# Kernel tuning notes

Hardware: AMD Instinct MI355X
Metric: run time of the kernel (lower is better)

Reference implementation:

```python
import jax, jax.numpy as jnp
import numpy as np
import math

D_MODEL = 2048
D_STATE = 64
D_CONV = 4
EXPAND = 2
HEADDIM = 128
NGROUPS = 1
CHUNK = 256
D_INNER = EXPAND * D_MODEL            # 4096
NHEADS = D_INNER // HEADDIM           # 32
CONV_DIM = D_INNER + 2 * NGROUPS * D_STATE   # 4224
D_IN_PROJ = 2 * D_INNER + 2 * NGROUPS * D_STATE + NHEADS  # 8352
BATCH, SEQLEN = 2, 4096
EPS = 1e-5


def segsum(x):
    # x: (..., T) -> (..., T, T) with s[i, j] = sum_{k=j+1}^{i} x[k], -inf above diag
    T = x.shape[-1]
    xx = jnp.broadcast_to(x[..., :, None], x.shape + (T,))
    mask_lo = jnp.tril(jnp.ones((T, T), dtype=bool), -1)
    xx = jnp.where(mask_lo, xx, 0.0)
    s = jnp.cumsum(xx, axis=-2)
    mask = jnp.tril(jnp.ones((T, T), dtype=bool), 0)
    return jnp.where(mask, s, -jnp.inf)


def ssd(X, A, B, C, block_len):
    # X:(b,L,h,p)  A:(b,L,h)  B,C:(b,L,h,n)
    b, L, h, p = X.shape
    c = L // block_len
    X = X.reshape(b, c, block_len, h, p)
    A = A.reshape(b, c, block_len, h).transpose(0, 3, 1, 2)  # b h c l
    B = B.reshape(b, c, block_len, h, -1)
    C = C.reshape(b, c, block_len, h, -1)
    A_cumsum = jnp.cumsum(A, axis=-1)
    Lmat = jnp.exp(segsum(A))                                  # b h c l l
    Y_diag = jnp.einsum('bclhn,bcshn,bhcls,bcshp->bclhp', C, B, Lmat, X)
    decay_states = jnp.exp(A_cumsum[:, :, :, -1:] - A_cumsum)  # b h c l
    states = jnp.einsum('bclhn,bhcl,bclhp->bchpn', B, decay_states, X)
    init = jnp.zeros_like(states[:, :1])
    states = jnp.concatenate([init, states], axis=1)
    decay_chunk = jnp.exp(segsum(jnp.pad(A_cumsum[:, :, :, -1], ((0, 0), (0, 0), (1, 0)))))
    new_states = jnp.einsum('bhzc,bchpn->bzhpn', decay_chunk, states)
    states, final_state = new_states[:, :-1], new_states[:, -1]
    Y_off = jnp.einsum('bclhn,bchpn,bhcl->bclhp', C, states, jnp.exp(A_cumsum))
    Y = (Y_diag + Y_off).reshape(b, L, h, p)
    return Y, final_state


def causal_dwconv(x, w, b):
    # x:(B,L,C)  w:(C,K) depthwise kernel  b:(C,)  -> causal conv, length preserved
    C, K = w.shape
    y = jax.lax.conv_general_dilated(
        x.transpose(0, 2, 1), w[:, None, :], (1,), [(K - 1, 0)],
        feature_group_count=C)
    return y.transpose(0, 2, 1) + b


def setup_inputs() -> dict:
    key = jax.random.key(0)
    ks = jax.random.split(key, 8)
    u = jax.random.normal(ks[0], (BATCH, SEQLEN, D_MODEL), dtype=jnp.float32)
    W_in = jax.random.normal(ks[1], (D_MODEL, D_IN_PROJ), dtype=jnp.float32) / np.sqrt(D_MODEL)
    conv_w = jax.random.normal(ks[2], (CONV_DIM, D_CONV), dtype=jnp.float32) / np.sqrt(D_CONV)
    conv_b = jnp.zeros((CONV_DIM,), dtype=jnp.float32)
    # dt_bias init: inverse-softplus of dt sampled log-uniform in [dt_min, dt_max]
    dt_min, dt_max, dt_floor = 1e-3, 1e-1, 1e-4
    dt = jnp.exp(jax.random.uniform(ks[3], (NHEADS,)) * (math.log(dt_max) - math.log(dt_min)) + math.log(dt_min))
    dt = jnp.clip(dt, dt_floor)
    dt_bias = dt + jnp.log(-jnp.expm1(-dt))
    A_log = jnp.log(jax.random.uniform(ks[4], (NHEADS,), minval=1.0, maxval=16.0))
    D = jnp.ones((NHEADS,), dtype=jnp.float32)
    norm_w = jnp.ones((D_INNER,), dtype=jnp.float32)
    W_out = jax.random.normal(ks[5], (D_INNER, D_MODEL), dtype=jnp.float32) / np.sqrt(D_INNER)
    return {"u": u, "W_in": W_in, "conv_w": conv_w, "conv_b": conv_b,
            "dt_bias": dt_bias, "A_log": A_log, "D": D, "norm_w": norm_w, "W_out": W_out}


def reference(u, W_in, conv_w, conv_b, dt_bias, A_log, D, norm_w, W_out):
    batch, seqlen, _ = u.shape
    zxbcdt = u @ W_in                                   # (B,L,8352)
    z, xBC, dt = jnp.split(zxbcdt, [D_INNER, D_INNER + CONV_DIM], axis=-1)
    dt = jax.nn.softplus(dt + dt_bias)                  # (B,L,H)
    xBC = jax.nn.silu(causal_dwconv(xBC, conv_w, conv_b))
    x, B, C = jnp.split(xBC, [D_INNER, D_INNER + NGROUPS * D_STATE], axis=-1)
    x = x.reshape(batch, seqlen, NHEADS, HEADDIM)
    B = jnp.broadcast_to(B.reshape(batch, seqlen, NGROUPS, D_STATE), (batch, seqlen, NHEADS, D_STATE))
    C = jnp.broadcast_to(C.reshape(batch, seqlen, NGROUPS, D_STATE), (batch, seqlen, NHEADS, D_STATE))
    A = -jnp.exp(A_log)                                 # (H,)
    x_scaled = x * dt[..., None]
    A_dt = A * dt                                       # (B,L,H)
    y, _final = ssd(x_scaled, A_dt, B, C, CHUNK)
    y = y.reshape(batch, seqlen, D_INNER)
    x_flat = x.reshape(batch, seqlen, D_INNER)
    D_full = jnp.repeat(D, HEADDIM)
    y = y + x_flat * D_full
    # gated RMSNorm, norm AFTER gate (norm_before_gate=False)
    yg = y * jax.nn.silu(z)
    var = jnp.mean(yg * yg, axis=-1, keepdims=True)
    y = yg * jax.lax.rsqrt(var + EPS) * norm_w
    return y @ W_out
```

## Files before the change

kernel.cpp:

```cpp
#include <hip/hip_runtime.h>

typedef short s8v __attribute__((ext_vector_type(8)));
typedef float f4v __attribute__((ext_vector_type(4)));
typedef unsigned short bfu;

#define MFMA16 __builtin_amdgcn_mfma_f32_16x16x32_bf16

constexpr int kSEQ = 4096;
constexpr int kBL  = 8192;
constexpr int kDM  = 2048;
constexpr int kDP  = 8352;
constexpr int kDPpad = 8448;
constexpr int kDI  = 4096;
constexpr int kCV  = 4224;
constexpr int kXBC = 4256;
constexpr int kNH  = 32;
constexpr int kHD  = 128;
constexpr int kDS  = 64;
constexpr int kCH  = 256;

#if defined(__has_builtin)
#  if __has_builtin(__builtin_amdgcn_global_load_lds)
#    define HAS_GLD 1
#  endif
#endif
#ifndef HAS_GLD
#  define HAS_GLD 0
#endif

__device__ __forceinline__ void gld_lds16(const void* g, void* lbase, int lane){
#if HAS_GLD
  (void)lane;
  __builtin_amdgcn_global_load_lds(
      (const __attribute__((address_space(1))) void*)g,
      (__attribute__((address_space(3))) void*)lbase, 16, 0, 0);
#else
  *(uint4*)((char*)lbase + lane * 16) = *(const uint4*)g;
#endif
}

__device__ __forceinline__ bfu f2bf(float f){
  union { float f; unsigned u; } c; c.f = f;
  return (bfu)((c.u + 0x7fffu + ((c.u >> 16) & 1u)) >> 16);
}
__device__ __forceinline__ float bf2f(bfu s){
  union { unsigned u; float f; } c; c.u = ((unsigned)s) << 16;
  return c.f;
}

__device__ __forceinline__ s8v frag_ld(const char* lds, int rowbase, int kh, int lane){
  int r = rowbase + (lane & 15);
  int slot = (kh << 2) + (lane >> 4);
  return *(const s8v*)(lds + (((r << 3) + (slot ^ (r & 7))) << 4));
}

__global__ __launch_bounds__(256) void k_zero(bfu* __restrict__ p, int n){
  int i = blockIdx.x * 256 + threadIdx.x;
  if (i < n) p[i] = 0;
}

__global__ __launch_bounds__(256) void k_cvt(const float* __restrict__ s, bfu* __restrict__ d, int n8){
  int i = blockIdx.x * 256 + threadIdx.x;
  int stride = gridDim.x * 256;
  for (; i < n8; i += stride){
    const float4* sp = (const float4*)(s + (size_t)i * 8);
    float4 a = sp[0], b = sp[1];
    uint4 pk; bfu* pp = (bfu*)&pk;
    pp[0]=f2bf(a.x); pp[1]=f2bf(a.y); pp[2]=f2bf(a.z); pp[3]=f2bf(a.w);
    pp[4]=f2bf(b.x); pp[5]=f2bf(b.y); pp[6]=f2bf(b.z); pp[7]=f2bf(b.w);
    *(uint4*)(d + (size_t)i * 8) = pk;
  }
}

__global__ __launch_bounds__(256) void k_transpose(const float* __restrict__ src, bfu* __restrict__ dst, int R, int C){
  __shared__ float tile[32][33];
  int c0 = blockIdx.x * 32, r0 = blockIdx.y * 32;
  int tx = threadIdx.x, ty = threadIdx.y;
  #pragma unroll
  for (int i = ty; i < 32; i += 8){
    int r = r0 + i, cc = c0 + tx;
    tile[i][tx] = (r < R && cc < C) ? src[(size_t)r * C + cc] : 0.f;
  }
  __syncthreads();
  #pragma unroll
  for (int i = ty; i < 32; i += 8){
    int dr = c0 + i, dc = r0 + tx;
    if (dr < C && dc < R) dst[(size_t)dr * R + dc] = f2bf(tile[tx][i]);
  }
}

template<int MODE>
__global__ __launch_bounds__(512, 2) void k_gemm256(const bfu* __restrict__ A, const bfu* __restrict__ Bt,
                                                    float* __restrict__ outF, bfu* __restrict__ outZ,
                                                    bfu* __restrict__ outX, int tilesN, int N, int K){
  extern __shared__ char lds[];
  int t = threadIdx.x, lane = t & 63, wave = t >> 6;
  int wr = wave >> 2, wc = wave & 3;
  int nwg = gridDim.x;
  int bid = blockIdx.x;
  int cpx = nwg >> 3;
  int wg = (bid & 7) * cpx + (bid >> 3);
  int tmTile = wg / tilesN, tnTile = wg % tilesN;
  int tm = tmTile << 8, tn = tnTile << 8;
  const bfu* Ab = A + (size_t)tm * K;
  const bfu* Bb = Bt + (size_t)tn * K;

  #define AU(b,kh) ((b) * 65536 + (kh) * 16384)
  #define BU(b,kh) ((b) * 65536 + 32768 + (kh) * 16384)

  auto stage_unit = [&](const bfu* srcbase, int unitOfs, int kcol0){
    #pragma unroll
    for (int j = 0; j < 2; ++j){
      int lg = j * 512 + wave * 64 + lane;
      int r = lg >> 2;
      int s = (lg & 3) ^ ((r >> 1) & 3);
      gld_lds16(srcbase + (size_t)r * K + kcol0 + s * 8,
                lds + unitOfs + (j * 512 + wave * 64) * 16, lane);
    }
  };
  auto rd_frag = [&](int unitOfs, int rbase) -> s8v {
    int r = rbase + (lane & 15);
    int s = lane >> 4;
    int g = (r << 2) + (s ^ ((r >> 1) & 3));
    return *(const s8v*)(lds + unitOfs + (g << 4));
  };

  f4v acc[8][4];
  f4v zz = {0.f, 0.f, 0.f, 0.f};
  #pragma unroll
  for (int m = 0; m < 8; ++m)
    #pragma unroll
    for (int n = 0; n < 4; ++n) acc[m][n] = zz;

  int nt = K >> 6;
  stage_unit(Ab, AU(0,0), 0);
  stage_unit(Bb, BU(0,0), 0);
  stage_unit(Ab, AU(0,1), 32);
  stage_unit(Bb, BU(0,1), 32);
  __builtin_amdgcn_sched_barrier(0);
  asm volatile("s_waitcnt vmcnt(4)" ::: "memory");
  __builtin_amdgcn_sched_barrier(0);
  __builtin_amdgcn_s_barrier();
  __builtin_amdgcn_sched_barrier(0);

  #pragma unroll 1
  for (int tt = 0; tt < nt; ++tt){
    int cb = tt & 1, nb = cb ^ 1;
    int k0n = (tt + 1) << 6;
    bool more = (tt + 1 < nt);
    #pragma unroll
    for (int kh = 0; kh < 2; ++kh){
      if (more){
        stage_unit(Ab, AU(nb,kh), k0n + kh * 32);
        stage_unit(Bb, BU(nb,kh), k0n + kh * 32);
      }
      s8v af[8], bf[4];
      #pragma unroll
      for (int m = 0; m < 8; ++m) af[m] = rd_frag(AU(cb,kh), wr * 128 + m * 16);
      #pragma unroll
      for (int n = 0; n < 4; ++n) bf[n] = rd_frag(BU(cb,kh), wc * 64 + n * 16);
      __builtin_amdgcn_s_setprio(1);
      #pragma unroll
      for (int n = 0; n < 4; ++n)
        #pragma unroll
        for (int m = 0; m < 8; ++m)
          acc[m][n] = MFMA16(af[m], bf[n], acc[m][n], 0, 0, 0);
      __builtin_amdgcn_s_setprio(0);
      __builtin_amdgcn_sched_barrier(0);
      asm volatile("s_waitcnt vmcnt(4)" ::: "memory");
      __builtin_amdgcn_sched_barrier(0);
      __builtin_amdgcn_s_barrier();
      __builtin_amdgcn_sched_barrier(0);
    }
  }

  int r0 = (lane >> 4) << 2;
  if (MODE == 0){
    #pragma unroll
    for (int m = 0; m < 8; ++m)
      #pragma unroll
      for (int n = 0; n < 4; ++n)
        #pragma unroll
        for (int r = 0; r < 4; ++r){
          size_t rg = (size_t)(tm + wr * 128 + m * 16 + r0 + r);
          int cg = tn + wc * 64 + n * 16 + (lane & 15);
          outF[rg * N + cg] = acc[m][n][r];
        }
  } else {
    #pragma unroll
    for (int m = 0; m < 8; ++m)
      #pragma unroll
      for (int n = 0; n < 4; ++n){
        int col = wc * 64 + n * 16 + (lane & 15);
        int cs = col >> 3, cl = col & 7;
        #pragma unroll
        for (int r = 0; r < 4; ++r){
          int row = wr * 128 + m * 16 + r0 + r;
          *(bfu*)(lds + row * 512 + ((cs ^ (row & 7)) << 4) + cl * 2) = f2bf(acc[m][n][r]);
        }
      }
    __syncthreads();
    bfu* op; int ldo, cofs;
    if (tn < 4096){ op = outZ; ldo = 4096; cofs = 0; }
    else          { op = outX; ldo = kXBC; cofs = 4096; }
    int row = t >> 1, half = t & 1;
    bfu* baseo = op + (size_t)(tm + row) * ldo + (tn - cofs) + half * 128;
    #pragma unroll
    for (int i = 0; i < 16; ++i){
      int cg = tn + half * 128 + i * 8;
      if (cg < kDP){
        uint4 v = *(const uint4*)(lds + row * 512 + (((half * 16 + i) ^ (row & 7)) << 4));
        *(uint4*)(baseo + i * 8) = v;
      }
    }
  }
  #undef AU
  #undef BU
}

__global__ __launch_bounds__(256) void k_conv(const bfu* __restrict__ xbc, const float* __restrict__ cw,
    const float* __restrict__ cb, bfu* __restrict__ xT,
    bfu* __restrict__ B16o, bfu* __restrict__ BTo, bfu* __restrict__ C16o){
  int cht = blockIdx.x;
  int lt = blockIdx.y;
  int b = lt >> 6;
  int l0 = (lt & 63) << 6;
  int t = threadIdx.x;
  __shared__ float w[256];
  __shared__ float bias[64];
  __shared__ bfu in16[67][66];
  __shared__ bfu out16[64][66];
  if (t < 64) bias[t] = cb[cht * 64 + t];
  w[t] = cw[cht * 256 + t];
  int chbase = cht * 64;
  for (int i = t; i < 67 * 64; i += 256){
    int rrow = i >> 6, cc = i & 63;
    int l = l0 + rrow - 3;
    bfu hv = 0;
    if (l >= 0) hv = xbc[((size_t)b * kSEQ + l) * kXBC + chbase + cc];
    in16[rrow][cc] = hv;
  }
  __syncthreads();
  for (int i = t; i < 4096; i += 256){
    int lr = i >> 6, cc = i & 63;
    float acc = bias[cc];
    #pragma unroll
    for (int j = 0; j < 4; ++j)
      acc += bf2f(in16[lr + j][cc]) * w[cc * 4 + j];
    float sv = acc / (1.f + __expf(-acc));
    out16[lr][cc] = f2bf(sv);
  }
  __syncthreads();
  if (chbase >= 4096){
    for (int i = t; i < 4096; i += 256){
      int lr = i >> 6, cc = i & 63;
      size_t row = (size_t)b * kSEQ + l0 + lr;
      int ch = chbase + cc;
      bfu v = out16[lr][cc];
      if (ch < 4096 + kDS) B16o[row * kDS + (ch - 4096)] = v;
      else                 C16o[row * kDS + (ch - 4096 - kDS)] = v;
    }
  }
  if (chbase < 4096 + kDS){
    for (int i = t; i < 4096; i += 256){
      int cc = i >> 6, lr = i & 63;
      int ch = chbase + cc;
      int lg = l0 + lr;
      bfu v = out16[lr][cc];
      if (ch < 4096){
        int hh = ch >> 7, p = ch & 127;
        xT[(((size_t)b * kNH + hh) * kHD + p) * kSEQ + lg] = v;
      } else if (ch < 4096 + kDS){
        BTo[((size_t)b * kDS + (ch - 4096)) * kSEQ + lg] = v;
      }
    }
  }
}

__global__ __launch_bounds__(256) void k_dtscan(const bfu* __restrict__ xbc, const float* __restrict__ dt_bias,
    const float* __restrict__ A_log, float* __restrict__ dtf, float* __restrict__ acum){
  int bi = blockIdx.x;
  int h = bi & 31, c = (bi >> 5) & 15, b = bi >> 9;
  int t = threadIdx.x;
  size_t row = (size_t)b * kSEQ + c * kCH + t;
  float draw = bf2f(xbc[row * kXBC + kCV + h]) + dt_bias[h];
  float dt = (draw > 20.f) ? draw : log1pf(__expf(draw));
  dtf[row * kNH + h] = dt;
  float dA = -__expf(A_log[h]) * dt;
  __shared__ float s[256];
  s[t] = dA;
  __syncthreads();
  #pragma unroll
  for (int off = 1; off < 256; off <<= 1){
    float v = (t >= off) ? s[t - off] : 0.f;
    __syncthreads();
    s[t] += v;
    __syncthreads();
  }
  acum[(size_t)bi * 256 + t] = s[t];
}

__global__ __launch_bounds__(256) void k_states(const bfu* __restrict__ xT, const bfu* __restrict__ BT,
    const float* __restrict__ dtf, const float* __restrict__ acum, bfu* __restrict__ states){
  int bi = blockIdx.x;
  int h = bi & 31, c = (bi >> 5) & 15, b = bi >> 9;
  int t = threadIdx.x, lane = t & 63, wave = t >> 6;
  int wr = wave >> 1, wc = wave & 1;
  __shared__ uint4 ldsX4[1024];
  __shared__ uint4 ldsB4[512];
  __shared__ float dsv[256];
  char* ldsX = (char*)ldsX4;
  char* ldsB = (char*)ldsB4;
  float Atot = acum[(size_t)bi * 256 + 255];
  {
    size_t row = (size_t)b * kSEQ + c * kCH + t;
    dsv[t] = dtf[row * kNH + h] * __expf(Atot - acum[(size_t)bi * 256 + t]);
  }
  f4v zz = {0.f, 0.f, 0.f, 0.f};
  f4v acc[4][2];
  #pragma unroll
  for (int m = 0; m < 4; ++m){ acc[m][0] = zz; acc[m][1] = zz; }
  const bfu* xTp = xT + ((size_t)b * kNH + h) * kHD * kSEQ + c * kCH;
  const bfu* BTp = BT + (size_t)b * kDS * kSEQ + c * kCH;
  __syncthreads();
  for (int kb = 0; kb < 4; ++kb){
    #pragma unroll
    for (int it = 0; it < 4; ++it){
      int s = it * 256 + t;
      int row = s >> 3;
      int srcslot = (s & 7) ^ (row & 7);
      gld_lds16(xTp + (size_t)row * kSEQ + kb * 64 + srcslot * 8,
                ldsX + it * 4096 + wave * 1024, lane);
    }
    #pragma unroll
    for (int it = 0; it < 2; ++it){
      int cidx = it * 256 + t;
      int row = cidx >> 3, slot = cidx & 7;
      uint4 v = *(const uint4*)(BTp + (size_t)row * kSEQ + kb * 64 + slot * 8);
      bfu* hp = (bfu*)&v;
      #pragma unroll
      for (int j = 0; j < 8; ++j)
        hp[j] = f2bf(bf2f(hp[j]) * dsv[kb * 64 + slot * 8 + j]);
      *(uint4*)(ldsB + (((row << 3) + (slot ^ (row & 7))) << 4)) = v;
    }
    __syncthreads();
    s8v af[4][2], bb[2][2];
    #pragma unroll
    for (int m = 0; m < 4; ++m){
      af[m][0] = frag_ld(ldsX, wr * 64 + m * 16, 0, lane);
      af[m][1] = frag_ld(ldsX, wr * 64 + m * 16, 1, lane);
    }
    #pragma unroll
    for (int nf = 0; nf < 2; ++nf){
      bb[nf][0] = frag_ld(ldsB, wc * 32 + nf * 16, 0, lane);
      bb[nf][1] = frag_ld(ldsB, wc * 32 + nf * 16, 1, lane);
    }
    #pragma unroll
    for (int kh = 0; kh < 2; ++kh)
      #pragma unroll
      for (int m = 0; m < 4; ++m)
        #pragma unroll
        for (int nf = 0; nf < 2; ++nf)
          acc[m][nf] = MFMA16(af[m][kh], bb[nf][kh], acc[m][nf], 0, 0, 0);
    __syncthreads();
  }
  bfu* sp = states + (size_t)bi * 8192;
  int r0 = (lane >> 4) << 2;
  #pragma unroll
  for (int m = 0; m < 4; ++m)
    #pragma unroll
    for (int nf = 0; nf < 2; ++nf)
      #pragma unroll
      for (int r = 0; r < 4; ++r){
        int p = wr * 64 + m * 16 + r0 + r;
        int n = wc * 32 + nf * 16 + (lane & 15);
        sp[p * 64 + n] = f2bf(acc[m][nf][r]);
      }
}

__global__ __launch_bounds__(256) void k_scan(bfu* __restrict__ st, const float* __restrict__ acum){
  int bh = blockIdx.x;
  int b = bh >> 5, h = bh & 31;
  int t = threadIdx.x;
  float run[32];
  #pragma unroll
  for (int j = 0; j < 32; ++j) run[j] = 0.f;
  for (int c = 0; c < 16; ++c){
    size_t bi = (size_t)((b * 16 + c) * 32 + h);
    float eT = __expf(acum[bi * 256 + 255]);
    size_t base = bi * 8192;
    #pragma unroll
    for (int j = 0; j < 32; ++j){
      size_t idx = base + j * 256 + t;
      float sl = bf2f(st[idx]);
      st[idx] = f2bf(run[j]);
      run[j] = run[j] * eT + sl;
    }
  }
}

__global__ __launch_bounds__(256) void k_y(
    const bfu* __restrict__ xT, const bfu* __restrict__ Bm, const bfu* __restrict__ Cm,
    const bfu* __restrict__ SIs, const float* __restrict__ dtf, const float* __restrict__ acum,
    const bfu* __restrict__ z16, const float* __restrict__ Dp,
    bfu* __restrict__ y16)
{
  int bi = blockIdx.x;
  int h = bi & 31, c = (bi >> 5) & 15, b = bi >> 9;
  int ph = blockIdx.y;
  int t = threadIdx.x, lane = t & 63, wave = t >> 6;
  int wl = wave << 6;
  __shared__ uint4 ldsP4[2048];
  __shared__ uint4 ldsT4[512];
  __shared__ float acumS[256];
  __shared__ float dtS[256];
  char* ldsP = ((char*)ldsP4) + (wave << 13);
  char* ldsT = (char*)ldsT4;
  size_t rowbase = (size_t)b * kSEQ + c * kCH;
  acumS[t] = acum[(size_t)bi * 256 + t];
  dtS[t] = dtf[(rowbase + t) * kNH + h];
  const bfu* SIp = SIs + (size_t)bi * 8192 + (size_t)ph * 4096;
  #pragma unroll
  for (int it = 0; it < 2; ++it){
    int cidx = it * 256 + t;
    int row = cidx >> 3, slot = cidx & 7;
    uint4 v = *(const uint4*)(SIp + row * 64 + slot * 8);
    *(uint4*)(ldsT + (((row << 3) + (slot ^ (row & 7))) << 4)) = v;
  }
  const bfu* Cp = Cm + rowbase * kDS;
  s8v cf[4][2];
  #pragma unroll
  for (int m = 0; m < 4; ++m){
    cf[m][0] = *(const s8v*)(Cp + (size_t)(wl + m * 16 + (lane & 15)) * kDS + ((lane >> 4) << 3));
    cf[m][1] = *(const s8v*)(Cp + (size_t)(wl + m * 16 + (lane & 15)) * kDS + 32 + ((lane >> 4) << 3));
  }
  __syncthreads();
  float Arow[16];
  #pragma unroll
  for (int m = 0; m < 4; ++m)
    #pragma unroll
    for (int r = 0; r < 4; ++r)
      Arow[m * 4 + r] = acumS[wl + m * 16 + ((lane >> 4) << 2) + r];
  f4v acc[4][4];
  {
    s8v bfo[4][2];
    #pragma unroll
    for (int pf = 0; pf < 4; ++pf){
      bfo[pf][0] = frag_ld(ldsT, pf << 4, 0, lane);
      bfo[pf][1] = frag_ld(ldsT, pf << 4, 1, lane);
    }
    f4v zz = {0.f, 0.f, 0.f, 0.f};
    #pragma unroll
    for (int m = 0; m < 4; ++m)
      #pragma unroll
      for (int pf = 0; pf < 4; ++pf){
        f4v v = zz;
        v = MFMA16(cf[m][0], bfo[pf][0], v, 0, 0, 0);
        v = MFMA16(cf[m][1], bfo[pf][1], v, 0, 0, 0);
        #pragma unroll
        for (int r = 0; r < 4; ++r) v[r] *= __expf(Arow[m * 4 + r]);
        acc[m][pf] = v;
      }
  }
  const bfu* Bp = Bm + rowbase * kDS;
  const bfu* xTp = xT + (((size_t)b * kNH + h) * kHD + ph * 64) * kSEQ + c * kCH;
  #pragma unroll 1
  for (int sb = 0; sb < 4; ++sb){
    __syncthreads();
    #pragma unroll
    for (int it = 0; it < 2; ++it){
      int s = it * 256 + t;
      int row = s >> 3;
      int srcslot = (s & 7) ^ (row & 7);
      gld_lds16(xTp + (size_t)row * kSEQ + sb * 64 + srcslot * 8,
                ldsT + it * 4096 + wave * 1024, lane);
    }
    f4v sv[4][4];
    {
      s8v bsf[4][2];
      #pragma unroll
      for (int sf = 0; sf < 4; ++sf){
        bsf[sf][0] = *(const s8v*)(Bp + (size_t)(sb * 64 + sf * 16 + (lane & 15)) * kDS + ((lane >> 4) << 3));
        bsf[sf][1] = *(const s8v*)(Bp + (size_t)(sb * 64 + sf * 16 + (lane & 15)) * kDS + 32 + ((lane >> 4) << 3));
      }
      f4v zz = {0.f, 0.f, 0.f, 0.f};
      #pragma unroll
      for (int m = 0; m < 4; ++m)
        #pragma unroll
        for (int sf = 0; sf < 4; ++sf){
          f4v v = zz;
          v = MFMA16(cf[m][0], bsf[sf][0], v, 0, 0, 0);
          v = MFMA16(cf[m][1], bsf[sf][1], v, 0, 0, 0);
          sv[m][sf] = v;
        }
    }
    int scb = sb << 6;
    float As[4], dts_[4];
    #pragma unroll
    for (int sf = 0; sf < 4; ++sf){
      As[sf] = acumS[scb + sf * 16 + (lane & 15)];
      dts_[sf] = dtS[scb + sf * 16 + (lane & 15)];
    }
    #pragma unroll
    for (int m = 0; m < 4; ++m)
      #pragma unroll
      for (int sf = 0; sf < 4; ++sf)
        #pragma unroll
        for (int r = 0; r < 4; ++r){
          int rloc = m * 16 + ((lane >> 4) << 2) + r;
          int scl = sf * 16 + (lane & 15);
          float pv = 0.f;
          if (wl + rloc >= scb + scl)
            pv = sv[m][sf][r] * __expf(Arow[m * 4 + r] - As[sf]) * dts_[sf];
          *(bfu*)(ldsP + rloc * 128 + ((((scl >> 3) ^ (rloc & 7)) << 3) + (scl & 7)) * 2) = f2bf(pv);
        }
    __syncthreads();
    s8v xb[4][2];
    #pragma unroll
    for (int pf = 0; pf < 4; ++pf){
      xb[pf][0] = frag_ld(ldsT, pf << 4, 0, lane);
      xb[pf][1] = frag_ld(ldsT, pf << 4, 1, lane);
    }
    #pragma unroll
    for (int m = 0; m < 4; ++m){
      s8v pa0 = frag_ld(ldsP, m << 4, 0, lane);
      s8v pa1 = frag_ld(ldsP, m << 4, 1, lane);
      #pragma unroll
      for (int pf = 0; pf < 4; ++pf){
        acc[m][pf] = MFMA16(pa0, xb[pf][0], acc[m][pf], 0, 0, 0);
        acc[m][pf] = MFMA16(pa1, xb[pf][1], acc[m][pf], 0, 0, 0);
      }
    }
  }
  float Dh = Dp[h];
  #pragma unroll
  for (int m = 0; m < 4; ++m)
    #pragma unroll
    for (int pf = 0; pf < 4; ++pf)
      #pragma unroll
      for (int r = 0; r < 4; ++r){
        int lloc = wl + m * 16 + ((lane >> 4) << 2) + r;
        int ploc = (pf << 4) + (lane & 15);
        size_t rowg = rowbase + lloc;
        int cg = (h << 7) + (ph << 6) + ploc;
        float xv = bf2f(xTp[(size_t)ploc * kSEQ + lloc]);
        float zv = bf2f(z16[rowg * kDI + cg]);
        float yv = acc[m][pf][r] + xv * Dh;
        float sg = zv / (1.f + __expf(-zv));
        y16[rowg * kDI + cg] = f2bf(yv * sg);
      }
}

__global__ __launch_bounds__(256) void k_norm(bfu* y, const float* __restrict__ nw){
  int row = blockIdx.x;
  int t = threadIdx.x, lane = t & 63, wave = t >> 6;
  bfu* yp = y + (size_t)row * kDI;
  uint4 a = *(const uint4*)(yp + t * 8);
  uint4 b = *(const uint4*)(yp + 2048 + t * 8);
  const bfu* ap = (const bfu*)&a;
  const bfu* bp = (const bfu*)&b;
  float va[8], vb[8];
  float ss = 0.f;
  #pragma unroll
  for (int j = 0; j < 8; ++j){
    va[j] = bf2f(ap[j]); ss += va[j] * va[j];
    vb[j] = bf2f(bp[j]); ss += vb[j] * vb[j];
  }
  #pragma unroll
  for (int o = 32; o > 0; o >>= 1) ss += __shfl_down(ss, o, 64);
  __shared__ float red[4];
  if (lane == 0) red[wave] = ss;
  __syncthreads();
  float tot = red[0] + red[1] + red[2] + red[3];
  float rs = rsqrtf(tot * (1.f / 4096.f) + 1e-5f);
  uint4 oa, ob;
  bfu* oap = (bfu*)&oa; bfu* obp = (bfu*)&ob;
  #pragma unroll
  for (int j = 0; j < 8; ++j){
    oap[j] = f2bf(va[j] * rs * nw[t * 8 + j]);
    obp[j] = f2bf(vb[j] * rs * nw[2048 + t * 8 + j]);
  }
  *(uint4*)(yp + t * 8) = oa;
  *(uint4*)(yp + 2048 + t * 8) = ob;
}

extern "C" void kernel_launch(void* const* d_in, const int* in_sizes, int n_in,
                              void* d_out, int out_size, void* d_ws, size_t ws_size,
                              hipStream_t stream){
  (void)in_sizes; (void)n_in; (void)out_size; (void)ws_size;
  const float* u       = (const float*)d_in[0];
  const float* W_in    = (const float*)d_in[1];
  const float* conv_w  = (const float*)d_in[2];
  const float* conv_b  = (const float*)d_in[3];
  const float* dt_bias = (const float*)d_in[4];
  const float* A_log   = (const float*)d_in[5];
  const float* Dp      = (const float*)d_in[6];
  const float* norm_w  = (const float*)d_in[7];
  const float* W_out   = (const float*)d_in[8];
  char* ws = (char*)d_ws;

  const size_t o_z    = 0;
  const size_t o_xbc  = o_z   + (size_t)kBL * kDI * 2;
  const size_t o_u16  = o_xbc + (size_t)kBL * kXBC * 2;
  const size_t o_xT   = o_u16 + (size_t)kBL * kDM * 2;
  const size_t o_B16  = o_xT  + (size_t)kBL * kDI * 2;
  const size_t o_BT   = o_B16 + (size_t)kBL * kDS * 2;
  const size_t o_C16  = o_BT  + (size_t)kBL * kDS * 2;
  const size_t o_dtf  = o_C16 + (size_t)kBL * kDS * 2;
  const size_t o_acum = o_dtf + (size_t)kBL * kNH * 4;
  const size_t o_states = o_u16;
  const size_t o_woutT  = o_u16 + (size_t)1024 * 8192 * 2;
  const size_t o_winT   = o_xT;
  const size_t o_y16    = o_xbc;

  bfu* z16    = (bfu*)(ws + o_z);
  bfu* xbc    = (bfu*)(ws + o_xbc);
  bfu* u16    = (bfu*)(ws + o_u16);
  bfu* xT     = (bfu*)(ws + o_xT);
  bfu* B16    = (bfu*)(ws + o_B16);
  bfu* BT     = (bfu*)(ws + o_BT);
  bfu* C16    = (bfu*)(ws + o_C16);
  float* dtf  = (float*)(ws + o_dtf);
  float* acum = (float*)(ws + o_acum);
  bfu* statesS= (bfu*)(ws + o_states);
  bfu* woutT  = (bfu*)(ws + o_woutT);
  bfu* winT   = (bfu*)(ws + o_winT);
  bfu* y16    = (bfu*)(ws + o_y16);

  (void)hipFuncSetAttribute(reinterpret_cast<const void*>(&k_gemm256<2>),
                            hipFuncAttributeMaxDynamicSharedMemorySize, 131072);
  (void)hipFuncSetAttribute(reinterpret_cast<const void*>(&k_gemm256<0>),
                            hipFuncAttributeMaxDynamicSharedMemorySize, 131072);

  k_zero<<<(96 * kDM + 255) / 256, 256, 0, stream>>>(winT + (size_t)kDP * kDM, 96 * kDM);
  k_cvt<<<2048, 256, 0, stream>>>(u, u16, kBL * kDM / 8);
  k_transpose<<<dim3(kDP / 32, kDM / 32), dim3(32, 8), 0, stream>>>(W_in, winT, kDM, kDP);
  k_gemm256<2><<<(kDPpad / 256) * (kBL / 256), 512, 131072, stream>>>(u16, winT, nullptr, z16, xbc, kDPpad / 256, kDPpad, kDM);
  k_conv<<<dim3(kCV / 64, kBL / 64), 256, 0, stream>>>(xbc, conv_w, conv_b, xT, B16, BT, C16);
  k_dtscan<<<1024, 256, 0, stream>>>(xbc, dt_bias, A_log, dtf, acum);
  k_transpose<<<dim3(kDM / 32, kDI / 32), dim3(32, 8), 0, stream>>>(W_out, woutT, kDI, kDM);
  k_states<<<1024, 256, 0, stream>>>(xT, BT, dtf, acum, statesS);
  k_scan<<<64, 256, 0, stream>>>(statesS, acum);
  k_y<<<dim3(1024, 2), 256, 0, stream>>>(xT, B16, C16, statesS, dtf, acum, z16, Dp, y16);
  k_norm<<<kBL, 256, 0, stream>>>(y16, norm_w);
  k_gemm256<0><<<(kDM / 256) * (kBL / 256), 512, 131072, stream>>>(y16, woutT, (float*)d_out, nullptr, nullptr, kDM / 256, kDM, kDI);
}
```

Baseline: 868.5 us.

## Fold RMSNorm scale into output GEMM and D-skip into diagonal P matrix

The norm weight is folded into the transposed W_out, and the per-row rsqrt is applied in the output GEMM epilogue, so the norm kernel only computes row scales and no longer rewrites y. The D skip term is added on the diagonal of the intra-chunk P matrix, which removes the strided xT reload in the y epilogue. It also waits for all loads on the last GEMM iteration. Risks: D is now rounded through bf16 in P, which may change accuracy slightly.

```diff
diff --git a/kernel.cpp b/kernel.cpp
--- a/kernel.cpp
+++ b/kernel.cpp
@@ -72,7 +72,8 @@
   }
 }
 
-__global__ __launch_bounds__(256) void k_transpose(const float* __restrict__ src, bfu* __restrict__ dst, int R, int C){
+__global__ __launch_bounds__(256) void k_transpose(const float* __restrict__ src, bfu* __restrict__ dst,
+                                                   int R, int C, const float* __restrict__ scale){
   __shared__ float tile[32][33];
   int c0 = blockIdx.x * 32, r0 = blockIdx.y * 32;
   int tx = threadIdx.x, ty = threadIdx.y;
@@ -85,14 +86,19 @@
   #pragma unroll
   for (int i = ty; i < 32; i += 8){
     int dr = c0 + i, dc = r0 + tx;
-    if (dr < C && dc < R) dst[(size_t)dr * R + dc] = f2bf(tile[tx][i]);
+    if (dr < C && dc < R){
+      float v = tile[tx][i];
+      if (scale) v *= scale[dc];
+      dst[(size_t)dr * R + dc] = f2bf(v);
+    }
   }
 }
 
 template<int MODE>
 __global__ __launch_bounds__(512, 2) void k_gemm256(const bfu* __restrict__ A, const bfu* __restrict__ Bt,
                                                     float* __restrict__ outF, bfu* __restrict__ outZ,
-                                                    bfu* __restrict__ outX, int tilesN, int N, int K){
+                                                    bfu* __restrict__ outX, const float* __restrict__ rsv,
+                                                    int tilesN, int N, int K){
   extern __shared__ char lds[];
   int t = threadIdx.x, lane = t & 63, wave = t >> 6;
   int wr = wave >> 2, wc = wave & 3;
@@ -167,7 +173,8 @@
           acc[m][n] = MFMA16(af[m], bf[n], acc[m][n], 0, 0, 0);
       __builtin_amdgcn_s_setprio(0);
       __builtin_amdgcn_sched_barrier(0);
-      asm volatile("s_waitcnt vmcnt(4)" ::: "memory");
+      if (more) { asm volatile("s_waitcnt vmcnt(4)" ::: "memory"); }
+      else      { asm volatile("s_waitcnt vmcnt(0)" ::: "memory"); }
       __builtin_amdgcn_sched_barrier(0);
       __builtin_amdgcn_s_barrier();
       __builtin_amdgcn_sched_barrier(0);
@@ -176,15 +183,19 @@
 
   int r0 = (lane >> 4) << 2;
   if (MODE == 0){
+    float* rsl = (float*)lds;
+    if (t < 256) rsl[t] = rsv[tm + t];
+    __syncthreads();
     #pragma unroll
     for (int m = 0; m < 8; ++m)
       #pragma unroll
       for (int n = 0; n < 4; ++n)
         #pragma unroll
         for (int r = 0; r < 4; ++r){
-          size_t rg = (size_t)(tm + wr * 128 + m * 16 + r0 + r);
+          int rl = wr * 128 + m * 16 + r0 + r;
+          size_t rg = (size_t)(tm + rl);
           int cg = tn + wc * 64 + n * 16 + (lane & 15);
-          outF[rg * N + cg] = acc[m][n][r];
+          outF[rg * N + cg] = acc[m][n][r] * rsl[rl];
         }
   } else {
     #pragma unroll
@@ -462,6 +473,7 @@
         acc[m][pf] = v;
       }
   }
+  float Dh = Dp[h];
   const bfu* Bp = Bm + rowbase * kDS;
   const bfu* xTp = xT + (((size_t)b * kNH + h) * kHD + ph * 64) * kSEQ + c * kCH;
   #pragma unroll 1
@@ -509,9 +521,12 @@
         for (int r = 0; r < 4; ++r){
           int rloc = m * 16 + ((lane >> 4) << 2) + r;
           int scl = sf * 16 + (lane & 15);
+          int d = (wl + rloc) - (scb + scl);
           float pv = 0.f;
-          if (wl + rloc >= scb + scl)
+          if (d >= 0)
             pv = sv[m][sf][r] * __expf(Arow[m * 4 + r] - As[sf]) * dts_[sf];
+          if (d == 0)
+            pv += Dh;
           *(bfu*)(ldsP + rloc * 128 + ((((scl >> 3) ^ (rloc & 7)) << 3) + (scl & 7)) * 2) = f2bf(pv);
         }
     __syncthreads();
@@ -532,7 +547,6 @@
       }
     }
   }
-  float Dh = Dp[h];
   #pragma unroll
   for (int m = 0; m < 4; ++m)
     #pragma unroll
@@ -543,45 +557,35 @@
         int ploc = (pf << 4) + (lane & 15);
         size_t rowg = rowbase + lloc;
         int cg = (h << 7) + (ph << 6) + ploc;
-        float xv = bf2f(xTp[(size_t)ploc * kSEQ + lloc]);
         float zv = bf2f(z16[rowg * kDI + cg]);
-        float yv = acc[m][pf][r] + xv * Dh;
         float sg = zv / (1.f + __expf(-zv));
-        y16[rowg * kDI + cg] = f2bf(yv * sg);
-      }
-}
-
-__global__ __launch_bounds__(256) void k_norm(bfu* y, const float* __restrict__ nw){
+        y16[rowg * kDI + cg] = f2bf(acc[m][pf][r] * sg);
+      }
+}
+
+__global__ __launch_bounds__(256) void k_rms(const bfu* __restrict__ y, float* __restrict__ rs){
   int row = blockIdx.x;
   int t = threadIdx.x, lane = t & 63, wave = t >> 6;
-  bfu* yp = y + (size_t)row * kDI;
+  const bfu* yp = y + (size_t)row * kDI;
   uint4 a = *(const uint4*)(yp + t * 8);
   uint4 b = *(const uint4*)(yp + 2048 + t * 8);
   const bfu* ap = (const bfu*)&a;
   const bfu* bp = (const bfu*)&b;
-  float va[8], vb[8];
   float ss = 0.f;
   #pragma unroll
   for (int j = 0; j < 8; ++j){
-    va[j] = bf2f(ap[j]); ss += va[j] * va[j];
-    vb[j] = bf2f(bp[j]); ss += vb[j] * vb[j];
+    float va = bf2f(ap[j]); ss += va * va;
+    float vb = bf2f(bp[j]); ss += vb * vb;
   }
   #pragma unroll
   for (int o = 32; o > 0; o >>= 1) ss += __shfl_down(ss, o, 64);
   __shared__ float red[4];
   if (lane == 0) red[wave] = ss;
   __syncthreads();
-  float tot = red[0] + red[1] + red[2] + red[3];
-  float rs = rsqrtf(tot * (1.f / 4096.f) + 1e-5f);
-  uint4 oa, ob;
-  bfu* oap = (bfu*)&oa; bfu* obp = (bfu*)&ob;
-  #pragma unroll
-  for (int j = 0; j < 8; ++j){
-    oap[j] = f2bf(va[j] * rs * nw[t * 8 + j]);
-    obp[j] = f2bf(vb[j] * rs * nw[2048 + t * 8 + j]);
-  }
-  *(uint4*)(yp + t * 8) = oa;
-  *(uint4*)(yp + 2048 + t * 8) = ob;
+  if (t == 0){
+    float tot = red[0] + red[1] + red[2] + red[3];
+    rs[row] = rsqrtf(tot * (1.f / 4096.f) + 1e-5f);
+  }
 }
 
 extern "C" void kernel_launch(void* const* d_in, const int* in_sizes, int n_in,
@@ -608,6 +612,7 @@
   const size_t o_C16  = o_BT  + (size_t)kBL * kDS * 2;
   const size_t o_dtf  = o_C16 + (size_t)kBL * kDS * 2;
   const size_t o_acum = o_dtf + (size_t)kBL * kNH * 4;
+  const size_t o_rs   = o_acum + (size_t)1024 * 256 * 4;
   const size_t o_states = o_u16;
   const size_t o_woutT  = o_u16 + (size_t)1024 * 8192 * 2;
   const size_t o_winT   = o_xT;
@@ -622,6 +627,7 @@
   bfu* C16    = (bfu*)(ws + o_C16);
   float* dtf  = (float*)(ws + o_dtf);
   float* acum = (float*)(ws + o_acum);
+  float* rs   = (float*)(ws + o_rs);
   bfu* statesS= (bfu*)(ws + o_states);
   bfu* woutT  = (bfu*)(ws + o_woutT);
   bfu* winT   = (bfu*)(ws + o_winT);
@@ -634,14 +640,14 @@
 
   k_zero<<<(96 * kDM + 255) / 256, 256, 0, stream>>>(winT + (size_t)kDP * kDM, 96 * kDM);
   k_cvt<<<2048, 256, 0, stream>>>(u, u16, kBL * kDM / 8);
-  k_transpose<<<dim3(kDP / 32, kDM / 32), dim3(32, 8), 0, stream>>>(W_in, winT, kDM, kDP);
-  k_gemm256<2><<<(kDPpad / 256) * (kBL / 256), 512, 131072, stream>>>(u16, winT, nullptr, z16, xbc, kDPpad / 256, kDPpad, kDM);
+  k_transpose<<<dim3(kDP / 32, kDM / 32), dim3(32, 8), 0, stream>>>(W_in, winT, kDM, kDP, nullptr);
+  k_gemm256<2><<<(kDPpad / 256) * (kBL / 256), 512, 131072, stream>>>(u16, winT, nullptr, z16, xbc, nullptr, kDPpad / 256, kDPpad, kDM);
   k_conv<<<dim3(kCV / 64, kBL / 64), 256, 0, stream>>>(xbc, conv_w, conv_b, xT, B16, BT, C16);
   k_dtscan<<<1024, 256, 0, stream>>>(xbc, dt_bias, A_log, dtf, acum);
-  k_transpose<<<dim3(kDM / 32, kDI / 32), dim3(32, 8), 0, stream>>>(W_out, woutT, kDI, kDM);
+  k_transpose<<<dim3(kDM / 32, kDI / 32), dim3(32, 8), 0, stream>>>(W_out, woutT, kDI, kDM, norm_w);
   k_states<<<1024, 256, 0, stream>>>(xT, BT, dtf, acum, statesS);
   k_scan<<<64, 256, 0, stream>>>(statesS, acum);
   k_y<<<dim3(1024, 2), 256, 0, stream>>>(xT, B16, C16, statesS, dtf, acum, z16, Dp, y16);
-  k_norm<<<kBL, 256, 0, stream>>>(y16, norm_w);
-  k_gemm256<0><<<(kDM / 256) * (kBL / 256), 512, 131072, stream>>>(y16, woutT, (float*)d_out, nullptr, nullptr, kDM / 256, kDM, kDI);
-}
+  k_rms<<<kBL, 256, 0, stream>>>(y16, rs);
+  k_gemm256<0><<<(kDM / 256) * (kBL / 256), 512, 131072, stream>>>(y16, woutT, (float*)d_out, nullptr, nullptr, rs, kDM / 256, kDM, kDI);
+}
```

After: 857.2 us. No clear change (-1.3%).
